# Kernel tuning notes

Measured on AMD Instinct MI355X. Metric: run time of the kernel, lower is better.

Reference implementation:

```python
import jax, jax.numpy as jnp
import numpy as np

N = 50000        # nodes
E = 800000       # edges (avg degree 16)
HIDDEN = 256
HEADS = 8
HEAD_DIM = HIDDEN // HEADS


def _linear_params(key, fan_in, fan_out):
    k1, k2 = jax.random.split(key)
    s = 1.0 / np.sqrt(fan_in)
    W = jax.random.uniform(k1, (fan_in, fan_out), jnp.float32, -s, s)
    b = jax.random.uniform(k2, (fan_out,), jnp.float32, -s, s)
    return W, b


def setup_inputs() -> dict:
    key = jax.random.key(0)
    ks = jax.random.split(key, 7)
    h = jax.random.normal(ks[0], (N, HIDDEN), jnp.float32)
    # sparse adjacency nonzeros: row = destination node, col = source node
    row = jnp.sort(jax.random.randint(ks[1], (E,), 0, N))
    col = jax.random.randint(ks[2], (E,), 0, N)
    Wq, bq = _linear_params(ks[3], HIDDEN, HIDDEN)
    Wk, bk = _linear_params(ks[4], HIDDEN, HIDDEN)
    Wv, bv = _linear_params(ks[5], HIDDEN, HIDDEN)
    Wo, bo = _linear_params(ks[6], HIDDEN, HIDDEN)
    return dict(h=h, row=row, col=col, Wq=Wq, bq=bq, Wk=Wk, bk=bk,
                Wv=Wv, bv=bv, Wo=Wo, bo=bo)


def reference(h, row, col, Wq, bq, Wk, bk, Wv, bv, Wo, bo):
    n = h.shape[0]
    scaling = HEAD_DIM ** (-0.5)
    q = ((h @ Wq + bq).reshape(n, HEADS, HEAD_DIM)) * scaling
    k = (h @ Wk + bk).reshape(n, HEADS, HEAD_DIM)
    v = (h @ Wv + bv).reshape(n, HEADS, HEAD_DIM)

    # bsddmm: per-edge, per-head sampled dot product q[dst] . k[src] -> [E, H]
    s = jnp.einsum('ehd,ehd->eh', q[row], k[col])

    # sparse row-wise softmax over each destination node's incoming edges
    m = jax.ops.segment_max(s, row, num_segments=n)          # [N, H]
    p = jnp.exp(s - m[row])                                   # [E, H]
    denom = jax.ops.segment_sum(p, row, num_segments=n)      # [N, H]
    attn = p / denom[row]                                     # [E, H]

    # bspmm: out[dst] = sum over incoming edges attn * v[src] -> [N, H, D]
    out = jax.ops.segment_sum(attn[:, :, None] * v[col], row, num_segments=n)
    return out.reshape(n, HIDDEN) @ Wo + bo
```

## Files before the change

kernel.cpp:

```cpp
#include <hip/hip_runtime.h>
#include <math.h>


typedef __attribute__((ext_vector_type(8))) short bf16x8;
typedef __attribute__((ext_vector_type(4))) float f32x4;
typedef __attribute__((ext_vector_type(2))) float f32x2;

__device__ __forceinline__ ushort f2bf(float f) {
    uint u = __float_as_uint(f);
    u += 0x7fffu + ((u >> 16) & 1u);
    return (ushort)(u >> 16);
}
__device__ __forceinline__ float bflo(uint u) { return __uint_as_float(u << 16); }
__device__ __forceinline__ float bfhi(uint u) { return __uint_as_float(u & 0xffff0000u); }

__device__ __forceinline__ uchar f2fp8(float f) {
    return (uchar)(__builtin_amdgcn_cvt_pk_fp8_f32(f, f, 0, false) & 0xff);
}
__device__ __forceinline__ void fp8x4_to_f32(uint u, float* f) {
    f32x2 lo = __builtin_amdgcn_cvt_pk_f32_fp8(u, false);
    f32x2 hi = __builtin_amdgcn_cvt_pk_f32_fp8(u, true);
    f[0] = lo[0]; f[1] = lo[1]; f[2] = hi[0]; f[3] = hi[1];
}

__device__ __forceinline__ void load_lds16(const void* g, void* l) {
    __builtin_amdgcn_global_load_lds(
        (const __attribute__((address_space(1))) void*)g,
        (__attribute__((address_space(3))) void*)l, 16, 0, 0);
}

__global__ __launch_bounds__(256) void convert_bf16(
    const float* __restrict__ in, ushort* __restrict__ out, size_t nelem)
{
    size_t i = ((size_t)blockIdx.x * 256 + threadIdx.x) * 4;
    if (i >= nelem) return;
    float4 v = *(const float4*)(in + i);
    *(ushort4*)(out + i) = make_ushort4(f2bf(v.x), f2bf(v.y), f2bf(v.z), f2bf(v.w));
}

__global__ __launch_bounds__(256) void prep(
    const float* __restrict__ Wq, const float* __restrict__ Wk,
    const float* __restrict__ Wv, const float* __restrict__ Wo,
    const float* __restrict__ bq, const float* __restrict__ bk,
    const float* __restrict__ bv,
    const int* __restrict__ row, int* __restrict__ row_ptr, int n, int E,
    ushort* __restrict__ Wall, ushort* __restrict__ Wot,
    float* __restrict__ ball)
{
    int m = blockIdx.y;
    if (m == 4) {
        int i = blockIdx.x * 256 + threadIdx.x;
        if (i > n) return;
        int lo = 0, hi = E;
        while (lo < hi) {
            int mid = (lo + hi) >> 1;
            if (row[mid] < i) lo = mid + 1; else hi = mid;
        }
        row_ptr[i] = lo;
        return;
    }
    if (blockIdx.x < 256) {
        int idx = blockIdx.x * 256 + threadIdx.x;
        int k = idx >> 8, nn = idx & 255;
        if (m < 3) {
            const float* W = m == 0 ? Wq : (m == 1 ? Wk : Wv);
            Wall[((size_t)m * 256 + nn) * 256 + k] = f2bf(W[idx]);
        } else {
            Wot[nn * 256 + k] = f2bf(Wo[idx]);
        }
    } else if (m < 3) {
        int i = threadIdx.x;
        ball[m * 256 + i] = (m == 0 ? bq : (m == 1 ? bk : bv))[i];
    }
}

template<int MODE>
__global__ __launch_bounds__(256) void gemm_mfma_lds(
    const ushort* __restrict__ A, const ushort* __restrict__ Wt,
    const float* __restrict__ bias, ushort* __restrict__ qb,
    uchar* __restrict__ kv, float* __restrict__ outf, int n, float scale)
{
    __shared__ ushort SH[2 * 128 * 64];
    ushort* As = SH;
    ushort* Bs = SH + 128 * 64;

    const int nwg = gridDim.x * gridDim.y;
    const int orig = blockIdx.y * gridDim.x + blockIdx.x;
    const int xcd = orig & 7, rnd = orig >> 3;
    const int q8 = nwg >> 3, r8 = nwg & 7;
    const int wgid = (xcd < r8 ? xcd * (q8 + 1) : r8 * (q8 + 1) + (xcd - r8) * q8) + rnd;
    const int tx = wgid % gridDim.x;
    const int ty = wgid / gridDim.x;

    const int tid = threadIdx.x;
    const int lane = tid & 63;
    const int wave = tid >> 6;
    const int col0 = tx * 128;
    const int row0 = ty * 128;
    const int fr = lane & 15;
    const int kg = lane >> 4;
    const int wr = (wave >> 1) * 64;
    const int wc = (wave & 1) * 64;

    f32x4 acc[4][4] = {};

    const int srow = tid >> 3;
    const int sc8 = tid & 7;

    for (int kt = 0; kt < 4; ++kt) {
        #pragma unroll
        for (int it = 0; it < 4; ++it) {
            int r = srow + it * 32;
            int chunk = sc8 ^ (r & 7);
            int ar = row0 + r; ar = ar < n ? ar : n - 1;
            load_lds16((const char*)A + (size_t)ar * 512 + kt * 128 + chunk * 16,
                       (char*)As + (it * 256 + tid) * 16);
            load_lds16((const char*)Wt + (size_t)(col0 + r) * 512 + kt * 128 + chunk * 16,
                       (char*)Bs + (it * 256 + tid) * 16);
        }
        __syncthreads();

        #pragma unroll
        for (int ks = 0; ks < 2; ++ks) {
            bf16x8 a[4], b[4];
            #pragma unroll
            for (int i = 0; i < 4; ++i) {
                int r = wr + i * 16 + fr;
                int chunk = (ks * 4 + kg) ^ (r & 7);
                a[i] = *(const bf16x8*)((const char*)As + r * 128 + chunk * 16);
            }
            #pragma unroll
            for (int j = 0; j < 4; ++j) {
                int c = wc + j * 16 + fr;
                int chunk = (ks * 4 + kg) ^ (c & 7);
                b[j] = *(const bf16x8*)((const char*)Bs + c * 128 + chunk * 16);
            }
            #pragma unroll
            for (int i = 0; i < 4; ++i)
                #pragma unroll
                for (int j = 0; j < 4; ++j)
                    acc[i][j] = __builtin_amdgcn_mfma_f32_16x16x32_bf16(
                        a[i], b[j], acc[i][j], 0, 0, 0);
        }
        __syncthreads();
    }

    if constexpr (MODE == 1) {
        #pragma unroll
        for (int j = 0; j < 4; ++j) {
            int gcol = col0 + wc + j * 16 + fr;
            float bj = bias[gcol];
            #pragma unroll
            for (int i = 0; i < 4; ++i) {
                #pragma unroll
                for (int r = 0; r < 4; ++r) {
                    int grow = row0 + wr + i * 16 + kg * 4 + r;
                    if (grow >= n) continue;
                    outf[(size_t)grow * 256 + gcol] = acc[i][j][r] + bj;
                }
            }
        }
        return;
    }

    char* sb = (char*)SH;
    const bool isf8 = (col0 >= 256 && col0 < 512);
    const bool isv  = (col0 >= 512);
    const float sc = (col0 < 256) ? scale : 1.f;

    #pragma unroll
    for (int j = 0; j < 4; ++j) {
        int cw = wc + j * 16 + fr;
        float bj = bias[col0 + cw];
        #pragma unroll
        for (int i = 0; i < 4; ++i) {
            #pragma unroll
            for (int r2 = 0; r2 < 4; ++r2) {
                int lrow = wr + i * 16 + kg * 4 + r2;
                float val = (acc[i][j][r2] + bj) * sc;
                if (isf8) {
                    int u = cw >> 4;
                    sb[lrow * 128 + ((u ^ (lrow & 7)) << 4) + (cw & 15)] = f2fp8(val);
                } else {
                    int u = cw >> 3;
                    *(ushort*)(sb + lrow * 256 + ((u ^ (lrow & 7)) << 4) +
                               ((cw & 7) << 1)) = f2bf(val);
                }
            }
        }
    }
    __syncthreads();

    if (isf8) {
        int seg = col0 - 256;
        #pragma unroll
        for (int pass = 0; pass < 4; ++pass) {
            int g = pass * 256 + tid;
            int lrow = g >> 3, u = g & 7;
            uint4 d = *(const uint4*)(sb + lrow * 128 + ((u ^ (lrow & 7)) << 4));
            int grow = row0 + lrow;
            if (grow < n)
                *(uint4*)((char*)kv + (size_t)grow * 544 + seg + u * 16) = d;
        }
    } else if (isv) {
        int vseg = col0 - 512;
        #pragma unroll
        for (int pass = 0; pass < 2; ++pass) {
            int t = pass * 256 + tid;
            int lrow = t >> 2, hh = t & 3;
            float vals[32];
            #pragma unroll
            for (int uu = 0; uu < 4; ++uu) {
                int u = hh * 4 + uu;
                uint4 d = *(const uint4*)(sb + lrow * 256 + ((u ^ (lrow & 7)) << 4));
                vals[uu*8+0] = bflo(d.x); vals[uu*8+1] = bfhi(d.x);
                vals[uu*8+2] = bflo(d.y); vals[uu*8+3] = bfhi(d.y);
                vals[uu*8+4] = bflo(d.z); vals[uu*8+5] = bfhi(d.z);
                vals[uu*8+6] = bflo(d.w); vals[uu*8+7] = bfhi(d.w);
            }
            float mx = 0.f;
            #pragma unroll
            for (int i = 0; i < 32; ++i) mx = fmaxf(mx, fabsf(vals[i]));
            float inv = mx > 0.f ? 127.f / mx : 0.f;
            float scl = mx > 0.f ? mx * (1.f / 127.f) : 0.f;
            uint pk[8];
            #pragma unroll
            for (int w = 0; w < 8; ++w) {
                uint b0 = (uint)(__float2int_rn(vals[w*4+0] * inv) + 128);
                uint b1 = (uint)(__float2int_rn(vals[w*4+1] * inv) + 128);
                uint b2 = (uint)(__float2int_rn(vals[w*4+2] * inv) + 128);
                uint b3 = (uint)(__float2int_rn(vals[w*4+3] * inv) + 128);
                pk[w] = b0 | (b1 << 8) | (b2 << 16) | (b3 << 24);
            }
            int grow = row0 + lrow;
            if (grow < n) {
                char* dst = (char*)kv + (size_t)grow * 544 + 256 + vseg + hh * 32;
                *(uint4*)dst        = make_uint4(pk[0], pk[1], pk[2], pk[3]);
                *(uint4*)(dst + 16) = make_uint4(pk[4], pk[5], pk[6], pk[7]);
                *(float*)((char*)kv + (size_t)grow * 544 + 512 +
                          ((vseg >> 5) + hh) * 4) = scl;
            }
        }
    } else {
        #pragma unroll
        for (int pass = 0; pass < 8; ++pass) {
            int g = pass * 256 + tid;
            int lrow = g >> 4, u = g & 15;
            uint4 d = *(const uint4*)(sb + lrow * 256 + ((u ^ (lrow & 7)) << 4));
            int grow = row0 + lrow;
            if (grow < n)
                *(uint4*)((char*)qb + (size_t)grow * 512 + col0 * 2 + u * 16) = d;
        }
    }
}

__global__ __launch_bounds__(256) void fused_attn(
    const ushort* __restrict__ qb, const uchar* __restrict__ kv,
    const int* __restrict__ col, const int* __restrict__ row_ptr,
    ushort* __restrict__ agg, int n)
{
    int node = blockIdx.x * 4 + (threadIdx.x >> 6);
    if (node >= n) return;
    int lane = threadIdx.x & 63;
    int p0 = row_ptr[node], p1 = row_ptr[node + 1];

    const int slot = lane >> 4;
    const int l16 = lane & 15;
    const int qoff = l16 * 32;

    float qf[16];
    {
        const char* qbp = (const char*)qb + (size_t)node * 512 + qoff;
        uint4 q0 = *(const uint4*)qbp;
        uint4 q1 = *(const uint4*)(qbp + 16);
        qf[0] = bflo(q0.x); qf[1] = bfhi(q0.x);
        qf[2] = bflo(q0.y); qf[3] = bfhi(q0.y);
        qf[4] = bflo(q0.z); qf[5] = bfhi(q0.z);
        qf[6] = bflo(q0.w); qf[7] = bfhi(q0.w);
        qf[8] = bflo(q1.x); qf[9] = bfhi(q1.x);
        qf[10] = bflo(q1.y); qf[11] = bfhi(q1.y);
        qf[12] = bflo(q1.z); qf[13] = bfhi(q1.z);
        qf[14] = bflo(q1.w); qf[15] = bfhi(q1.w);
    }

    float denom = 0.f;
    float cacc = 0.f;
    float acc[16] = {};

#define ISSUE(IDX, K, V, S)                                                    \
    do {                                                                       \
        int src_ = __shfl(cl, (IDX));                                          \
        const char* b_ = (const char*)kv + (size_t)src_ * 544;                 \
        K = *(const uint4*)(b_ + l16 * 16);                                    \
        V = *(const uint4*)(b_ + 256 + l16 * 16);                              \
        S = *(const float*)(b_ + 512 + ((l16 >> 1) << 2));                     \
    } while (0)

#define CONSUME(VALID, K, V, S)                                                \
    do {                                                                       \
        float kf_[16];                                                         \
        fp8x4_to_f32(K.x, kf_); fp8x4_to_f32(K.y, kf_ + 4);                    \
        fp8x4_to_f32(K.z, kf_ + 8); fp8x4_to_f32(K.w, kf_ + 12);               \
        float sp_ = 0.f;                                                       \
        _Pragma("unroll")                                                      \
        for (int i_ = 0; i_ < 16; ++i_) sp_ = fmaf(qf[i_], kf_[i_], sp_);      \
        float s_ = sp_ + __shfl_xor(sp_, 1);                                   \
        float p_ = (VALID) ? __expf(s_) : 0.f;                                 \
        denom += p_;                                                           \
        float ps_ = p_ * (S);                                                  \
        cacc += ps_;                                                           \
        uint w_;                                                               \
        w_ = V.x;                                                              \
        acc[0]  = fmaf(ps_, (float)(w_ & 0xff),         acc[0]);               \
        acc[1]  = fmaf(ps_, (float)((w_ >> 8) & 0xff),  acc[1]);               \
        acc[2]  = fmaf(ps_, (float)((w_ >> 16) & 0xff), acc[2]);               \
        acc[3]  = fmaf(ps_, (float)(w_ >> 24),          acc[3]);               \
        w_ = V.y;                                                              \
        acc[4]  = fmaf(ps_, (float)(w_ & 0xff),         acc[4]);               \
        acc[5]  = fmaf(ps_, (float)((w_ >> 8) & 0xff),  acc[5]);               \
        acc[6]  = fmaf(ps_, (float)((w_ >> 16) & 0xff), acc[6]);               \
        acc[7]  = fmaf(ps_, (float)(w_ >> 24),          acc[7]);               \
        w_ = V.z;                                                              \
        acc[8]  = fmaf(ps_, (float)(w_ & 0xff),         acc[8]);               \
        acc[9]  = fmaf(ps_, (float)((w_ >> 8) & 0xff),  acc[9]);               \
        acc[10] = fmaf(ps_, (float)((w_ >> 16) & 0xff), acc[10]);              \
        acc[11] = fmaf(ps_, (float)(w_ >> 24),          acc[11]);              \
        w_ = V.w;                                                              \
        acc[12] = fmaf(ps_, (float)(w_ & 0xff),         acc[12]);              \
        acc[13] = fmaf(ps_, (float)((w_ >> 8) & 0xff),  acc[13]);              \
        acc[14] = fmaf(ps_, (float)((w_ >> 16) & 0xff), acc[14]);              \
        acc[15] = fmaf(ps_, (float)(w_ >> 24),          acc[15]);              \
    } while (0)

    for (int bbase = p0; bbase < p1; bbase += 64) {
        int bd = min(64, p1 - bbase);
        int cl = (lane < bd) ? col[bbase + lane] : 0;
        int nch = (bd + 3) >> 2;

        uint4 kA, vA, kB, vB; float sA, sB;
        ISSUE(slot, kA, vA, sA);
        int c = 0;
        for (;;) {
            if (c + 1 < nch) ISSUE((c + 1) * 4 + slot, kB, vB, sB);
            CONSUME(c * 4 + slot < bd, kA, vA, sA);
            if (++c >= nch) break;
            if (c + 1 < nch) ISSUE((c + 1) * 4 + slot, kA, vA, sA);
            CONSUME(c * 4 + slot < bd, kB, vB, sB);
            if (++c >= nch) break;
        }
    }
#undef ISSUE
#undef CONSUME

    #pragma unroll
    for (int i = 0; i < 16; ++i) acc[i] = fmaf(-128.f, cacc, acc[i]);
    #pragma unroll
    for (int i = 0; i < 16; ++i) {
        acc[i] += __shfl_xor(acc[i], 16);
        acc[i] += __shfl_xor(acc[i], 32);
    }
    denom += __shfl_xor(denom, 16);
    denom += __shfl_xor(denom, 32);

    if (slot == 0) {
        float inv = denom > 0.f ? 1.f / denom : 0.f;
        uint o[8];
        #pragma unroll
        for (int i = 0; i < 8; ++i)
            o[i] = (uint)f2bf(acc[2 * i] * inv) |
                   ((uint)f2bf(acc[2 * i + 1] * inv) << 16);
        char* ob = (char*)agg + (size_t)node * 512 + qoff;
        *(uint4*)ob        = make_uint4(o[0], o[1], o[2], o[3]);
        *(uint4*)(ob + 16) = make_uint4(o[4], o[5], o[6], o[7]);
    }
}

extern "C" void kernel_launch(void* const* d_in, const int* in_sizes, int n_in,
                              void* d_out, int out_size, void* d_ws, size_t ws_size,
                              hipStream_t stream)
{
    const float* h  = (const float*)d_in[0];
    const int*   row = (const int*)d_in[1];
    const int*   col = (const int*)d_in[2];
    const float* Wq = (const float*)d_in[3];
    const float* bq = (const float*)d_in[4];
    const float* Wk = (const float*)d_in[5];
    const float* bk = (const float*)d_in[6];
    const float* Wv = (const float*)d_in[7];
    const float* bv = (const float*)d_in[8];
    const float* Wo = (const float*)d_in[9];
    const float* bo = (const float*)d_in[10];
    float* out = (float*)d_out;

    const int n = in_sizes[0] / 256;
    const int E = in_sizes[1];
    const size_t NC = (size_t)n * 256;

    char* base = (char*)d_ws;
    ushort* qbb  = (ushort*)(base);
    uchar*  kv   = (uchar*)(base + NC * 2);
    char*   p2   = base + NC * 2 + (size_t)n * 544;
    ushort* hb   = (ushort*)(p2);
    ushort* aggb = (ushort*)(p2 + NC * 2);
    ushort* Wall = (ushort*)(p2 + NC * 4);
    ushort* Wot  = Wall + 768 * 256;
    float*  ball = (float*)(Wot + 65536);
    int* row_ptr = (int*)(ball + 768);

    const float scaling = 0.17677669529663687f;

    dim3 blk(256);
    prep<<<dim3(257, 5), blk, 0, stream>>>(Wq, Wk, Wv, Wo, bq, bk, bv,
                                           row, row_ptr, n, E,
                                           Wall, Wot, ball);
    convert_bf16<<<dim3((int)((NC / 4 + 255) / 256)), blk, 0, stream>>>(h, hb, NC);

    const int mtiles = (n + 127) / 128;
    gemm_mfma_lds<0><<<dim3(6, mtiles), blk, 0, stream>>>(
        hb, Wall, ball, qbb, kv, nullptr, n, scaling);

    fused_attn<<<dim3((n + 3) / 4), blk, 0, stream>>>(
        qbb, kv, col, row_ptr, aggb, n);

    gemm_mfma_lds<1><<<dim3(2, mtiles), blk, 0, stream>>>(
        aggb, Wot, bo, nullptr, nullptr, out, n, 1.f);
}
```

Measured before the change: 158.9 us.

## Fuse fp32-to-bf16 conversion into QKV GEMM loads and split V scales out

Removes the separate convert_bf16 kernel: the QKV GEMM now reads fp32 h directly, converts each chunk to bf16 in registers and stores it to LDS, in place of the async global-to-LDS copy. This saves one launch and a full write plus re-read of the bf16 copy of h. The per-row V scales move out of the 544-byte kv record into a separate vscale array, so each record is a 512-byte aligned row. The cost is that h is now read as fp32 by each of the 6 column tiles instead of once, and the A loads become synchronous register loads, so they may overlap less with compute.

```diff
diff --git a/kernel.cpp b/kernel.cpp
--- a/kernel.cpp
+++ b/kernel.cpp
@@ -27,15 +27,6 @@
     __builtin_amdgcn_global_load_lds(
         (const __attribute__((address_space(1))) void*)g,
         (__attribute__((address_space(3))) void*)l, 16, 0, 0);
-}
-
-__global__ __launch_bounds__(256) void convert_bf16(
-    const float* __restrict__ in, ushort* __restrict__ out, size_t nelem)
-{
-    size_t i = ((size_t)blockIdx.x * 256 + threadIdx.x) * 4;
-    if (i >= nelem) return;
-    float4 v = *(const float4*)(in + i);
-    *(ushort4*)(out + i) = make_ushort4(f2bf(v.x), f2bf(v.y), f2bf(v.z), f2bf(v.w));
 }
 
 __global__ __launch_bounds__(256) void prep(
@@ -76,9 +67,10 @@
 
 template<int MODE>
 __global__ __launch_bounds__(256) void gemm_mfma_lds(
-    const ushort* __restrict__ A, const ushort* __restrict__ Wt,
+    const void* __restrict__ Av, const ushort* __restrict__ Wt,
     const float* __restrict__ bias, ushort* __restrict__ qb,
-    uchar* __restrict__ kv, float* __restrict__ outf, int n, float scale)
+    uchar* __restrict__ kv, float* __restrict__ vscale,
+    float* __restrict__ outf, int n, float scale)
 {
     __shared__ ushort SH[2 * 128 * 64];
     ushort* As = SH;
@@ -113,9 +105,22 @@
             int r = srow + it * 32;
             int chunk = sc8 ^ (r & 7);
             int ar = row0 + r; ar = ar < n ? ar : n - 1;
-            load_lds16((const char*)A + (size_t)ar * 512 + kt * 128 + chunk * 16,
-                       (char*)As + (it * 256 + tid) * 16);
-            load_lds16((const char*)Wt + (size_t)(col0 + r) * 512 + kt * 128 + chunk * 16,
+            if constexpr (MODE == 0) {
+                const float4* hp = (const float4*)((const char*)Av +
+                    (size_t)ar * 1024 + kt * 256 + chunk * 32);
+                float4 f0 = hp[0], f1 = hp[1];
+                uint4 w;
+                w.x = (uint)f2bf(f0.x) | ((uint)f2bf(f0.y) << 16);
+                w.y = (uint)f2bf(f0.z) | ((uint)f2bf(f0.w) << 16);
+                w.z = (uint)f2bf(f1.x) | ((uint)f2bf(f1.y) << 16);
+                w.w = (uint)f2bf(f1.z) | ((uint)f2bf(f1.w) << 16);
+                *(uint4*)((char*)As + (it * 256 + tid) * 16) = w;
+            } else {
+                load_lds16((const char*)Av + (size_t)ar * 512 + kt * 128 + chunk * 16,
+                           (char*)As + (it * 256 + tid) * 16);
+            }
+            load_lds16((const char*)Wt + (size_t)(col0 + srow + it * 32) * 512 +
+                           kt * 128 + chunk * 16,
                        (char*)Bs + (it * 256 + tid) * 16);
         }
         __syncthreads();
@@ -200,7 +205,7 @@
             uint4 d = *(const uint4*)(sb + lrow * 128 + ((u ^ (lrow & 7)) << 4));
             int grow = row0 + lrow;
             if (grow < n)
-                *(uint4*)((char*)kv + (size_t)grow * 544 + seg + u * 16) = d;
+                *(uint4*)((char*)kv + (size_t)grow * 512 + seg + u * 16) = d;
         }
     } else if (isv) {
         int vseg = col0 - 512;
@@ -234,11 +239,10 @@
             }
             int grow = row0 + lrow;
             if (grow < n) {
-                char* dst = (char*)kv + (size_t)grow * 544 + 256 + vseg + hh * 32;
+                char* dst = (char*)kv + (size_t)grow * 512 + 256 + vseg + hh * 32;
                 *(uint4*)dst        = make_uint4(pk[0], pk[1], pk[2], pk[3]);
                 *(uint4*)(dst + 16) = make_uint4(pk[4], pk[5], pk[6], pk[7]);
-                *(float*)((char*)kv + (size_t)grow * 544 + 512 +
-                          ((vseg >> 5) + hh) * 4) = scl;
+                vscale[(size_t)grow * 8 + (vseg >> 5) + hh] = scl;
             }
         }
     } else {
@@ -256,8 +260,8 @@
 
 __global__ __launch_bounds__(256) void fused_attn(
     const ushort* __restrict__ qb, const uchar* __restrict__ kv,
-    const int* __restrict__ col, const int* __restrict__ row_ptr,
-    ushort* __restrict__ agg, int n)
+    const float* __restrict__ vscale, const int* __restrict__ col,
+    const int* __restrict__ row_ptr, ushort* __restrict__ agg, int n)
 {
     int node = blockIdx.x * 4 + (threadIdx.x >> 6);
     if (node >= n) return;
@@ -290,10 +294,10 @@
 #define ISSUE(IDX, K, V, S)                                                    \
     do {                                                                       \
         int src_ = __shfl(cl, (IDX));                                          \
-        const char* b_ = (const char*)kv + (size_t)src_ * 544;                 \
+        const char* b_ = (const char*)kv + (size_t)src_ * 512;                 \
         K = *(const uint4*)(b_ + l16 * 16);                                    \
         V = *(const uint4*)(b_ + 256 + l16 * 16);                              \
-        S = *(const float*)(b_ + 512 + ((l16 >> 1) << 2));                     \
+        S = vscale[(size_t)src_ * 8 + (l16 >> 1)];                             \
     } while (0)
 
 #define CONSUME(VALID, K, V, S)                                                \
@@ -397,15 +401,14 @@
     const size_t NC = (size_t)n * 256;
 
     char* base = (char*)d_ws;
-    ushort* qbb  = (ushort*)(base);
-    uchar*  kv   = (uchar*)(base + NC * 2);
-    char*   p2   = base + NC * 2 + (size_t)n * 544;
-    ushort* hb   = (ushort*)(p2);
-    ushort* aggb = (ushort*)(p2 + NC * 2);
-    ushort* Wall = (ushort*)(p2 + NC * 4);
-    ushort* Wot  = Wall + 768 * 256;
-    float*  ball = (float*)(Wot + 65536);
-    int* row_ptr = (int*)(ball + 768);
+    ushort* qbb    = (ushort*)(base);
+    uchar*  kv     = (uchar*)(base + NC * 2);
+    float*  vscale = (float*)(base + NC * 4);
+    ushort* aggb   = (ushort*)(base + NC * 4 + (size_t)n * 32);
+    ushort* Wall   = (ushort*)(base + NC * 6 + (size_t)n * 32);
+    ushort* Wot    = Wall + 768 * 256;
+    float*  ball   = (float*)(Wot + 65536);
+    int* row_ptr   = (int*)(ball + 768);
 
     const float scaling = 0.17677669529663687f;
 
@@ -413,15 +416,14 @@
     prep<<<dim3(257, 5), blk, 0, stream>>>(Wq, Wk, Wv, Wo, bq, bk, bv,
                                            row, row_ptr, n, E,
                                            Wall, Wot, ball);
-    convert_bf16<<<dim3((int)((NC / 4 + 255) / 256)), blk, 0, stream>>>(h, hb, NC);
 
     const int mtiles = (n + 127) / 128;
     gemm_mfma_lds<0><<<dim3(6, mtiles), blk, 0, stream>>>(
-        hb, Wall, ball, qbb, kv, nullptr, n, scaling);
+        h, Wall, ball, qbb, kv, vscale, nullptr, n, scaling);
 
     fused_attn<<<dim3((n + 3) / 4), blk, 0, stream>>>(
-        qbb, kv, col, row_ptr, aggb, n);
+        qbb, kv, vscale, col, row_ptr, aggb, n);
 
     gemm_mfma_lds<1><<<dim3(2, mtiles), blk, 0, stream>>>(
-        aggb, Wot, bo, nullptr, nullptr, out, n, 1.f);
-}
+        aggb, Wot, bo, nullptr, nullptr, nullptr, out, n, 1.f);
+}
```

Result: slower. 166.7 us (+4.9%).
